# Performance work log

Hardware: AMD Instinct MI355X
Metric: run time of the kernel (lower is better)

The kernel has to match this reference:

```python
import jax, jax.numpy as jnp
import numpy as np

EMB = 1024
HEADS = 16
HEAD_DIM = EMB // HEADS


def setup_inputs() -> dict:
    key = jax.random.key(0)
    ks = jax.random.split(key, 9)
    B, T = 2, 2048
    s = 1.0 / np.sqrt(EMB)
    x = jax.random.normal(ks[0], (B, T, EMB), dtype=jnp.float32)
    Wq = jax.random.normal(ks[1], (EMB, EMB), dtype=jnp.float32) * s
    bq = jnp.zeros((EMB,), dtype=jnp.float32)
    Wk = jax.random.normal(ks[2], (EMB, EMB), dtype=jnp.float32) * s
    bk = jnp.zeros((EMB,), dtype=jnp.float32)
    Wv = jax.random.normal(ks[3], (EMB, EMB), dtype=jnp.float32) * s
    bv = jnp.zeros((EMB,), dtype=jnp.float32)
    Wo = jax.random.normal(ks[4], (EMB, EMB), dtype=jnp.float32) * s
    bo = jnp.zeros((EMB,), dtype=jnp.float32)
    return {"x": x, "Wq": Wq, "bq": bq, "Wk": Wk, "bk": bk,
            "Wv": Wv, "bv": bv, "Wo": Wo, "bo": bo}


def reference(x, Wq, bq, Wk, bk, Wv, bv, Wo, bo):
    B, T, C = x.shape
    H, D = HEADS, HEAD_DIM
    # QKV projections -> (B, H, T, D)
    q = (x @ Wq + bq).reshape(B, T, H, D).transpose(0, 2, 1, 3)
    k = (x @ Wk + bk).reshape(B, T, H, D).transpose(0, 2, 1, 3)
    v = (x @ Wv + bv).reshape(B, T, H, D).transpose(0, 2, 1, 3)
    scores = jnp.einsum('bhqd,bhkd->bhqk', q, k) / np.sqrt(D).astype(np.float32)
    causal = jnp.tril(jnp.ones((T, T), dtype=bool))  # True where allowed
    scores = jnp.where(causal, scores, -jnp.inf)
    weights = jax.nn.softmax(scores, axis=-1)  # dropout is identity at eval
    out = jnp.einsum('bhqk,bhkd->bhqd', weights, v)
    out = out.transpose(0, 2, 1, 3).reshape(B, T, C)
    return out @ Wo + bo
```

## Files before the change

### kernel.cpp

```cpp
#include <hip/hip_runtime.h>

typedef unsigned short u16;
typedef u16 u16x8 __attribute__((ext_vector_type(8)));
typedef __bf16 bf16x8 __attribute__((ext_vector_type(8)));
typedef float f32x4 __attribute__((ext_vector_type(4)));

#define EMB 1024
#define TT 2048
#define BB 2
#define NHEADS 16
#define HD 64
#define MTOT (BB * TT)

__device__ __forceinline__ u16 cvt(float f) {
  return __builtin_bit_cast(u16, (__bf16)f);
}

__device__ __forceinline__ bf16x8 asbf(u16x8 v) {
  return __builtin_bit_cast(bf16x8, v);
}

__device__ __forceinline__ void gload16(const void* g, void* l) {
  __builtin_amdgcn_global_load_lds(
      (const __attribute__((address_space(1))) void*)g,
      (__attribute__((address_space(3))) void*)l, 16, 0, 0);
}

__global__ __launch_bounds__(256) void k_prep(
    const float* __restrict__ x, u16* __restrict__ xb,
    const float* __restrict__ W0, const float* __restrict__ W1,
    const float* __restrict__ W2, const float* __restrict__ W3,
    u16* __restrict__ T0, u16* __restrict__ T1, u16* __restrict__ T2,
    u16* __restrict__ T3) {
  __shared__ float tile[32][33];
  const int bid = blockIdx.x;
  const int tid = threadIdx.x;
  if (bid >= 4096) {
    int i = (bid - 4096) * 256 + tid;
    float4 a = ((const float4*)x)[i * 2];
    float4 b = ((const float4*)x)[i * 2 + 1];
    u16x8 o;
    o[0] = cvt(a.x); o[1] = cvt(a.y); o[2] = cvt(a.z); o[3] = cvt(a.w);
    o[4] = cvt(b.x); o[5] = cvt(b.y); o[6] = cvt(b.z); o[7] = cvt(b.w);
    ((u16x8*)xb)[i] = o;
    return;
  }
  const int z = bid >> 10;
  const float* __restrict__ W = (z == 0) ? W0 : (z == 1) ? W1 : (z == 2) ? W2 : W3;
  u16* __restrict__ Wt = (z == 0) ? T0 : (z == 1) ? T1 : (z == 2) ? T2 : T3;
  const int b = bid & 1023;
  const int bx = (b & 31) * 32, by = (b >> 5) * 32;
  const int tx = tid & 31;
  const int ty = tid >> 5;
#pragma unroll
  for (int r = ty; r < 32; r += 8) tile[r][tx] = W[(by + r) * EMB + bx + tx];
  __syncthreads();
  const int tx2 = tid & 15;
  const int ty2 = tid >> 4;
#pragma unroll
  for (int r = ty2; r < 32; r += 16) {
    unsigned v = (unsigned)cvt(tile[2 * tx2][r]) |
                 ((unsigned)cvt(tile[2 * tx2 + 1][r]) << 16);
    *(unsigned*)&Wt[(bx + r) * EMB + by + 2 * tx2] = v;
  }
}

__global__ __launch_bounds__(256) void k_gemm_qkv(
    const u16* __restrict__ xb, const u16* __restrict__ WqT,
    const u16* __restrict__ WkT, const u16* __restrict__ WvT,
    const float* __restrict__ bq, const float* __restrict__ bk,
    const float* __restrict__ bv, u16* __restrict__ Q, u16* __restrict__ K,
    u16* __restrict__ Vt) {
  __shared__ u16 Al[128 * 64];
  __shared__ u16 Bl[128 * 64];
  const int tid = threadIdx.x;
  const int lane = tid & 63;
  const int w = tid >> 6;
  const int wr = w >> 1, wc = w & 1;
  const int lr = lane & 15, lg = lane >> 4;
  const int m0 = blockIdx.x * 128;
  const int nb = blockIdx.y;
  const int seg = nb >> 3;
  const int n0 = (nb & 7) * 128;
  const u16* __restrict__ Bt = (seg == 0) ? WqT : (seg == 1) ? WkT : WvT;
  const float* __restrict__ bias = (seg == 0) ? bq : (seg == 1) ? bk : bv;

  f32x4 acc[4][4];
#pragma unroll
  for (int i = 0; i < 4; i++)
#pragma unroll
    for (int j = 0; j < 4; j++) acc[i][j] = (f32x4){0.f, 0.f, 0.f, 0.f};

  const int srow = tid >> 3;
  const int sgz = ((tid >> 3) & 3) | (((tid >> 6) & 1) << 2);
  const int sc = (tid & 7) ^ sgz;
  const u16* ga0 = xb + (m0 + srow) * EMB + sc * 8;
  const u16* gb0 = Bt + (n0 + srow) * EMB + sc * 8;
  char* la0 = (char*)Al + w * 1024;
  char* lb0 = (char*)Bl + w * 1024;
  const int gfr = (lr & 3) | (((lr >> 3) & 1) << 2);

  for (int k0 = 0; k0 < EMB; k0 += 64) {
#pragma unroll
    for (int m = 0; m < 4; m++) {
      gload16(ga0 + (32 * m) * EMB + k0, la0 + m * 4096);
      gload16(gb0 + (32 * m) * EMB + k0, lb0 + m * 4096);
    }
    __syncthreads();
    u16x8 af[4][2], bfr[4][2];
#pragma unroll
    for (int hh = 0; hh < 2; hh++) {
      const int pc = ((hh * 4 + lg) ^ gfr) * 16;
#pragma unroll
      for (int mi = 0; mi < 4; mi++)
        af[mi][hh] =
            *(const u16x8*)((char*)Al + (wr * 64 + mi * 16 + lr) * 128 + pc);
#pragma unroll
      for (int ni = 0; ni < 4; ni++)
        bfr[ni][hh] =
            *(const u16x8*)((char*)Bl + (wc * 64 + ni * 16 + lr) * 128 + pc);
    }
    if (seg == 2) {
#pragma unroll
      for (int hh = 0; hh < 2; hh++)
#pragma unroll
        for (int mi = 0; mi < 4; mi++)
#pragma unroll
          for (int ni = 0; ni < 4; ni++)
            acc[mi][ni] = __builtin_amdgcn_mfma_f32_16x16x32_bf16(
                asbf(af[mi][hh]), asbf(bfr[ni][hh]), acc[mi][ni], 0, 0, 0);
    } else {
#pragma unroll
      for (int hh = 0; hh < 2; hh++)
#pragma unroll
        for (int mi = 0; mi < 4; mi++)
#pragma unroll
          for (int ni = 0; ni < 4; ni++)
            acc[mi][ni] = __builtin_amdgcn_mfma_f32_16x16x32_bf16(
                asbf(bfr[ni][hh]), asbf(af[mi][hh]), acc[mi][ni], 0, 0, 0);
    }
    __syncthreads();
  }

  const int b = m0 >> 11;
  if (seg == 2) {
#pragma unroll
    for (int ni = 0; ni < 4; ni++) {
      const int n = n0 + wc * 64 + ni * 16 + lr;
      const float bv_ = bias[n];
      const int h = n >> 6, d = n & 63;
      u16* vrow = Vt + (((b * NHEADS + h) * HD) + d) * TT;
#pragma unroll
      for (int mi = 0; mi < 4; mi++) {
        const int t0 = (m0 + wr * 64 + mi * 16 + lg * 4) & 2047;
        ushort4 pk;
        pk.x = cvt(acc[mi][ni][0] + bv_);
        pk.y = cvt(acc[mi][ni][1] + bv_);
        pk.z = cvt(acc[mi][ni][2] + bv_);
        pk.w = cvt(acc[mi][ni][3] + bv_);
        *(ushort4*)&vrow[t0] = pk;
      }
    }
  } else {
    u16* __restrict__ dst = (seg == 0) ? Q : K;
    const float qs = 0.18033688011f;
#pragma unroll
    for (int ni = 0; ni < 4; ni++) {
      const int nbase = n0 + wc * 64 + ni * 16 + lg * 4;
      const float4 bv4 = *(const float4*)&bias[nbase];
      const int h = nbase >> 6, d0 = nbase & 63;
#pragma unroll
      for (int mi = 0; mi < 4; mi++) {
        const int t = (m0 + wr * 64 + mi * 16 + lr) & 2047;
        float v0 = acc[mi][ni][0] + bv4.x;
        float v1 = acc[mi][ni][1] + bv4.y;
        float v2 = acc[mi][ni][2] + bv4.z;
        float v3 = acc[mi][ni][3] + bv4.w;
        if (seg == 0) { v0 *= qs; v1 *= qs; v2 *= qs; v3 *= qs; }
        ushort4 pk;
        pk.x = cvt(v0); pk.y = cvt(v1); pk.z = cvt(v2); pk.w = cvt(v3);
        *(ushort4*)&dst[(((b * NHEADS + h) * TT) + t) * HD + d0] = pk;
      }
    }
  }
}

__global__ __launch_bounds__(512) void k_attn(const u16* __restrict__ Q,
                                              const u16* __restrict__ Kg,
                                              const u16* __restrict__ Vt,
                                              u16* __restrict__ AO) {
  __shared__ u16 Kl[2][64 * 64];
  __shared__ u16 Vl[2][64 * 64];
  const int tid = threadIdx.x;
  const int lane = tid & 63;
  const int w = tid >> 6;
  const int lr = lane & 15, lg = lane >> 4;
  const int bh = blockIdx.x;
  const int pair = blockIdx.y;
  const int lo = pair, hi = 31 - pair;
  const int qblk = (w < 4) ? hi : lo;
  const int myend = qblk;
  const int q0 = qblk * 64 + (w & 3) * 16;
  const u16* __restrict__ Qh = Q + bh * TT * HD;
  const u16* __restrict__ Kh = Kg + bh * TT * HD;
  const u16* __restrict__ Vh = Vt + bh * HD * TT;

  const int srow = tid >> 3;
  const int sgz = ((tid >> 3) & 3) | (((tid >> 6) & 1) << 2);
  const int sc = (tid & 7) ^ sgz;

  u16x8 qf[2];
  qf[0] = *(const u16x8*)&Qh[(q0 + lr) * HD + lg * 8];
  qf[1] = *(const u16x8*)&Qh[(q0 + lr) * HD + 32 + lg * 8];

  f32x4 accO[4];
#pragma unroll
  for (int i = 0; i < 4; i++) accO[i] = (f32x4){0.f, 0.f, 0.f, 0.f};
  float mst = -__builtin_inff();
  float lsum = 0.f;

  const int nkt = hi + 1;

  gload16(Kh + srow * HD + sc * 8, (char*)Kl[0] + w * 1024);
  gload16(Vh + srow * TT + sc * 8, (char*)Vl[0] + w * 1024);
  __syncthreads();

  for (int kt = 0; kt < nkt; ++kt) {
    const int k0 = kt * 64;
    const int cur = kt & 1;
    if (kt + 1 < nkt) {
      const int kn = k0 + 64;
      gload16(Kh + (kn + srow) * HD + sc * 8, (char*)Kl[cur ^ 1] + w * 1024);
      gload16(Vh + srow * TT + kn + sc * 8, (char*)Vl[cur ^ 1] + w * 1024);
    }
    if (kt <= myend) {
      const char* Kc = (const char*)Kl[cur];
      const char* Vc = (const char*)Vl[cur];

      f32x4 s[4];
#pragma unroll
      for (int n = 0; n < 4; n++) s[n] = (f32x4){0.f, 0.f, 0.f, 0.f};
      __builtin_amdgcn_s_setprio(1);
#pragma unroll
      for (int n = 0; n < 4; n++) {
        const int kr =
            (lr & 3) + ((n & 1) << 2) + ((lr >> 2) << 3) + ((n >> 1) << 5);
        const int gg = (kr & 3) | (((kr >> 3) & 1) << 2);
#pragma unroll
        for (int dh = 0; dh < 2; dh++) {
          const int bo = ((dh * 4 + lg) ^ gg) << 4;
          u16x8 kf = *(const u16x8*)(Kc + kr * 128 + bo);
          s[n] = __builtin_amdgcn_mfma_f32_16x16x32_bf16(asbf(kf), asbf(qf[dh]),
                                                         s[n], 0, 0, 0);
        }
      }
      __builtin_amdgcn_s_setprio(0);
      if (kt == myend) {
        const int rowq = q0 + lr;
#pragma unroll
        for (int n = 0; n < 4; n++) {
          const int cb = k0 + ((n & 1) << 2) + (lg << 3) + ((n >> 1) << 5);
#pragma unroll
          for (int r = 0; r < 4; r++)
            if (cb + r > rowq) s[n][r] = -__builtin_inff();
        }
      }
      float m01 = fmaxf(fmaxf(s[0][0], s[0][1]), fmaxf(s[0][2], s[0][3]));
      float m1 = fmaxf(fmaxf(s[1][0], s[1][1]), fmaxf(s[1][2], s[1][3]));
      float m2 = fmaxf(fmaxf(s[2][0], s[2][1]), fmaxf(s[2][2], s[2][3]));
      float m3 = fmaxf(fmaxf(s[3][0], s[3][1]), fmaxf(s[3][2], s[3][3]));
      float lmax = fmaxf(fmaxf(m01, m1), fmaxf(m2, m3));
      if (!__all(lmax - mst <= 11.0f)) {
        float rm = lmax;
        rm = fmaxf(rm, __shfl_xor(rm, 16));
        rm = fmaxf(rm, __shfl_xor(rm, 32));
        float mnew = fmaxf(mst, rm);
        float corr = exp2f(mst - mnew);
        lsum *= corr;
        mst = mnew;
#pragma unroll
        for (int r = 0; r < 4; r++) {
          float ca = __shfl(corr, 20 * lg + r);
#pragma unroll
          for (int dt = 0; dt < 4; dt++) accO[dt][r] *= ca;
        }
      }
      float p[4][4];
      float ls = 0.f;
#pragma unroll
      for (int n = 0; n < 4; n++)
#pragma unroll
        for (int r = 0; r < 4; r++) {
          p[n][r] = exp2f(s[n][r] - mst);
          ls += p[n][r];
        }
      lsum += ls;
      u16x8 a1, a2;
#pragma unroll
      for (int r = 0; r < 4; r++) {
        a1[r] = cvt(p[0][r]);
        a1[4 + r] = cvt(p[1][r]);
        a2[r] = cvt(p[2][r]);
        a2[4 + r] = cvt(p[3][r]);
      }
      __builtin_amdgcn_s_setprio(1);
#pragma unroll
      for (int dt = 0; dt < 4; dt++) {
        const int row = dt * 16 + lr;
        const int gg = (row & 3) | (((row >> 3) & 1) << 2);
        const int bo0 = ((lg ^ gg) << 4);
        const int bo1 = (((4 + lg) ^ gg) << 4);
        u16x8 vf0 = *(const u16x8*)(Vc + row * 128 + bo0);
        u16x8 vf1 = *(const u16x8*)(Vc + row * 128 + bo1);
        accO[dt] = __builtin_amdgcn_mfma_f32_16x16x32_bf16(asbf(a1), asbf(vf0),
                                                           accO[dt], 0, 0, 0);
        accO[dt] = __builtin_amdgcn_mfma_f32_16x16x32_bf16(asbf(a2), asbf(vf1),
                                                           accO[dt], 0, 0, 0);
      }
      __builtin_amdgcn_s_setprio(0);
    }
    __syncthreads();
  }
  float t = lsum;
  t += __shfl_xor(t, 16);
  t += __shfl_xor(t, 32);
  float rinv = 1.0f / t;
  float ra[4];
#pragma unroll
  for (int r = 0; r < 4; r++) ra[r] = __shfl(rinv, 20 * lg + r);
  const int b = bh >> 4, h = bh & 15;
#pragma unroll
  for (int dt = 0; dt < 4; dt++)
#pragma unroll
    for (int r = 0; r < 4; r++) {
      const int row = q0 + lg * 4 + r;
      const int d = h * 64 + dt * 16 + lr;
      AO[(b * TT + row) * EMB + d] = cvt(accO[dt][r] * ra[r]);
    }
}

__global__ __launch_bounds__(256) void k_gemm_out(const u16* __restrict__ AO,
                                                  const u16* __restrict__ WoT,
                                                  const float* __restrict__ bo,
                                                  float* __restrict__ out) {
  __shared__ u16 Al[128 * 64];
  __shared__ u16 Bl[128 * 64];
  const int tid = threadIdx.x;
  const int lane = tid & 63;
  const int w = tid >> 6;
  const int wr = w >> 1, wc = w & 1;
  const int lr = lane & 15, lg = lane >> 4;
  const int m0 = blockIdx.x * 128;
  const int n0 = blockIdx.y * 128;

  f32x4 acc[4][4];
#pragma unroll
  for (int i = 0; i < 4; i++)
#pragma unroll
    for (int j = 0; j < 4; j++) acc[i][j] = (f32x4){0.f, 0.f, 0.f, 0.f};

  const int srow = tid >> 3;
  const int sgz = ((tid >> 3) & 3) | (((tid >> 6) & 1) << 2);
  const int sc = (tid & 7) ^ sgz;
  const u16* ga0 = AO + (m0 + srow) * EMB + sc * 8;
  const u16* gb0 = WoT + (n0 + srow) * EMB + sc * 8;
  char* la0 = (char*)Al + w * 1024;
  char* lb0 = (char*)Bl + w * 1024;
  const int gfr = (lr & 3) | (((lr >> 3) & 1) << 2);

  for (int k0 = 0; k0 < EMB; k0 += 64) {
#pragma unroll
    for (int m = 0; m < 4; m++) {
      gload16(ga0 + (32 * m) * EMB + k0, la0 + m * 4096);
      gload16(gb0 + (32 * m) * EMB + k0, lb0 + m * 4096);
    }
    __syncthreads();
    u16x8 af[4][2], bfr[4][2];
#pragma unroll
    for (int hh = 0; hh < 2; hh++) {
      const int pc = ((hh * 4 + lg) ^ gfr) * 16;
#pragma unroll
      for (int mi = 0; mi < 4; mi++)
        af[mi][hh] =
            *(const u16x8*)((char*)Al + (wr * 64 + mi * 16 + lr) * 128 + pc);
#pragma unroll
      for (int ni = 0; ni < 4; ni++)
        bfr[ni][hh] =
            *(const u16x8*)((char*)Bl + (wc * 64 + ni * 16 + lr) * 128 + pc);
    }
#pragma unroll
    for (int hh = 0; hh < 2; hh++)
#pragma unroll
      for (int mi = 0; mi < 4; mi++)
#pragma unroll
        for (int ni = 0; ni < 4; ni++)
          acc[mi][ni] = __builtin_amdgcn_mfma_f32_16x16x32_bf16(
              asbf(bfr[ni][hh]), asbf(af[mi][hh]), acc[mi][ni], 0, 0, 0);
    __syncthreads();
  }

#pragma unroll
  for (int ni = 0; ni < 4; ni++) {
    const int nbase = n0 + wc * 64 + ni * 16 + lg * 4;
    const float4 bv4 = *(const float4*)&bo[nbase];
#pragma unroll
    for (int mi = 0; mi < 4; mi++) {
      const int m = m0 + wr * 64 + mi * 16 + lr;
      float4 v;
      v.x = acc[mi][ni][0] + bv4.x;
      v.y = acc[mi][ni][1] + bv4.y;
      v.z = acc[mi][ni][2] + bv4.z;
      v.w = acc[mi][ni][3] + bv4.w;
      *(float4*)&out[m * EMB + nbase] = v;
    }
  }
}

extern "C" void kernel_launch(void* const* d_in, const int* in_sizes, int n_in,
                              void* d_out, int out_size, void* d_ws,
                              size_t ws_size, hipStream_t stream) {
  const float* x = (const float*)d_in[0];
  const float* Wq = (const float*)d_in[1];
  const float* bq = (const float*)d_in[2];
  const float* Wk = (const float*)d_in[3];
  const float* bk = (const float*)d_in[4];
  const float* Wv = (const float*)d_in[5];
  const float* bv = (const float*)d_in[6];
  const float* Wo = (const float*)d_in[7];
  const float* bo = (const float*)d_in[8];
  float* out = (float*)d_out;

  char* ws = (char*)d_ws;
  u16* xb = (u16*)ws;
  u16* WqT = (u16*)(ws + (8u << 20));
  u16* WkT = (u16*)(ws + (10u << 20));
  u16* WvT = (u16*)(ws + (12u << 20));
  u16* WoT = (u16*)(ws + (14u << 20));
  u16* Qb = (u16*)(ws + (16u << 20));
  u16* Kb = (u16*)(ws + (24u << 20));
  u16* Vtb = (u16*)(ws + (32u << 20));
  u16* AO = xb;

  k_prep<<<6144, 256, 0, stream>>>(x, xb, Wq, Wk, Wv, Wo, WqT, WkT, WvT, WoT);
  k_gemm_qkv<<<dim3(32, 24), 256, 0, stream>>>(xb, WqT, WkT, WvT, bq, bk, bv,
                                               Qb, Kb, Vtb);
  k_attn<<<dim3(32, 16), 512, 0, stream>>>(Qb, Kb, Vtb, AO);
  k_gemm_out<<<dim3(32, 8), 256, 0, stream>>>(AO, WoT, bo, out);
}
```

Before: 132.4 us.

## Double-buffer QKV GEMM LDS tiles with BK=32 and drop swizzle

Restructures the QKV projection GEMM main loop so the next K-slice is prefetched into a second LDS buffer while MFMAs run on the current one. The K step drops from 64 to 32 and the XOR swizzle on the LDS layout is removed. The operand order is also unified, so Q/K results now come out transposed and are stored as scalar 2-byte writes instead of ushort4 vectors. This aims to hide global-load latency, but it risks LDS bank conflicts from the unswizzled layout, uncoalesced scalar stores in the Q/K epilogue, and more barriers per unit of work.

```diff
diff --git a/kernel.cpp b/kernel.cpp
--- a/kernel.cpp
+++ b/kernel.cpp
@@ -71,8 +71,8 @@
     const float* __restrict__ bq, const float* __restrict__ bk,
     const float* __restrict__ bv, u16* __restrict__ Q, u16* __restrict__ K,
     u16* __restrict__ Vt) {
-  __shared__ u16 Al[128 * 64];
-  __shared__ u16 Bl[128 * 64];
+  __shared__ u16 Al[2][128 * 32];
+  __shared__ u16 Bl[2][128 * 32];
   const int tid = threadIdx.x;
   const int lane = tid & 63;
   const int w = tid >> 6;
@@ -91,54 +91,40 @@
 #pragma unroll
     for (int j = 0; j < 4; j++) acc[i][j] = (f32x4){0.f, 0.f, 0.f, 0.f};
 
-  const int srow = tid >> 3;
-  const int sgz = ((tid >> 3) & 3) | (((tid >> 6) & 1) << 2);
-  const int sc = (tid & 7) ^ sgz;
-  const u16* ga0 = xb + (m0 + srow) * EMB + sc * 8;
-  const u16* gb0 = Bt + (n0 + srow) * EMB + sc * 8;
-  char* la0 = (char*)Al + w * 1024;
-  char* lb0 = (char*)Bl + w * 1024;
-  const int gfr = (lr & 3) | (((lr >> 3) & 1) << 2);
-
-  for (int k0 = 0; k0 < EMB; k0 += 64) {
-#pragma unroll
-    for (int m = 0; m < 4; m++) {
-      gload16(ga0 + (32 * m) * EMB + k0, la0 + m * 4096);
-      gload16(gb0 + (32 * m) * EMB + k0, lb0 + m * 4096);
-    }
-    __syncthreads();
-    u16x8 af[4][2], bfr[4][2];
-#pragma unroll
-    for (int hh = 0; hh < 2; hh++) {
-      const int pc = ((hh * 4 + lg) ^ gfr) * 16;
-#pragma unroll
-      for (int mi = 0; mi < 4; mi++)
-        af[mi][hh] =
-            *(const u16x8*)((char*)Al + (wr * 64 + mi * 16 + lr) * 128 + pc);
+  const int srow = tid >> 2;
+  const int scol = (tid & 3) * 8;
+  const u16* ga0 = xb + (m0 + srow) * EMB + scol;
+  const u16* gb0 = Bt + (n0 + srow) * EMB + scol;
+  const int lofs = w * 1024;
+
+  gload16(ga0, (char*)Al[0] + lofs);
+  gload16(ga0 + 64 * EMB, (char*)Al[0] + lofs + 4096);
+  gload16(gb0, (char*)Bl[0] + lofs);
+  gload16(gb0 + 64 * EMB, (char*)Bl[0] + lofs + 4096);
+  __syncthreads();
+
+  int cur = 0;
+  for (int k0 = 0; k0 < EMB; k0 += 32, cur ^= 1) {
+    if (k0 + 32 < EMB) {
+      const int kn = k0 + 32;
+      gload16(ga0 + kn, (char*)Al[cur ^ 1] + lofs);
+      gload16(ga0 + 64 * EMB + kn, (char*)Al[cur ^ 1] + lofs + 4096);
+      gload16(gb0 + kn, (char*)Bl[cur ^ 1] + lofs);
+      gload16(gb0 + 64 * EMB + kn, (char*)Bl[cur ^ 1] + lofs + 4096);
+    }
+    u16x8 af[4], bfr[4];
+#pragma unroll
+    for (int mi = 0; mi < 4; mi++)
+      af[mi] = *(const u16x8*)&Al[cur][(wr * 64 + mi * 16 + lr) * 32 + lg * 8];
+#pragma unroll
+    for (int ni = 0; ni < 4; ni++)
+      bfr[ni] = *(const u16x8*)&Bl[cur][(wc * 64 + ni * 16 + lr) * 32 + lg * 8];
+#pragma unroll
+    for (int mi = 0; mi < 4; mi++)
 #pragma unroll
       for (int ni = 0; ni < 4; ni++)
-        bfr[ni][hh] =
-            *(const u16x8*)((char*)Bl + (wc * 64 + ni * 16 + lr) * 128 + pc);
-    }
-    if (seg == 2) {
-#pragma unroll
-      for (int hh = 0; hh < 2; hh++)
-#pragma unroll
-        for (int mi = 0; mi < 4; mi++)
-#pragma unroll
-          for (int ni = 0; ni < 4; ni++)
-            acc[mi][ni] = __builtin_amdgcn_mfma_f32_16x16x32_bf16(
-                asbf(af[mi][hh]), asbf(bfr[ni][hh]), acc[mi][ni], 0, 0, 0);
-    } else {
-#pragma unroll
-      for (int hh = 0; hh < 2; hh++)
-#pragma unroll
-        for (int mi = 0; mi < 4; mi++)
-#pragma unroll
-          for (int ni = 0; ni < 4; ni++)
-            acc[mi][ni] = __builtin_amdgcn_mfma_f32_16x16x32_bf16(
-                asbf(bfr[ni][hh]), asbf(af[mi][hh]), acc[mi][ni], 0, 0, 0);
-    }
+        acc[mi][ni] = __builtin_amdgcn_mfma_f32_16x16x32_bf16(
+            asbf(af[mi]), asbf(bfr[ni]), acc[mi][ni], 0, 0, 0);
     __syncthreads();
   }
 
@@ -163,23 +149,21 @@
     }
   } else {
     u16* __restrict__ dst = (seg == 0) ? Q : K;
-    const float qs = 0.18033688011f;
-#pragma unroll
-    for (int ni = 0; ni < 4; ni++) {
-      const int nbase = n0 + wc * 64 + ni * 16 + lg * 4;
-      const float4 bv4 = *(const float4*)&bias[nbase];
-      const int h = nbase >> 6, d0 = nbase & 63;
-#pragma unroll
-      for (int mi = 0; mi < 4; mi++) {
-        const int t = (m0 + wr * 64 + mi * 16 + lr) & 2047;
-        float v0 = acc[mi][ni][0] + bv4.x;
-        float v1 = acc[mi][ni][1] + bv4.y;
-        float v2 = acc[mi][ni][2] + bv4.z;
-        float v3 = acc[mi][ni][3] + bv4.w;
-        if (seg == 0) { v0 *= qs; v1 *= qs; v2 *= qs; v3 *= qs; }
-        ushort4 pk;
-        pk.x = cvt(v0); pk.y = cvt(v1); pk.z = cvt(v2); pk.w = cvt(v3);
-        *(ushort4*)&dst[(((b * NHEADS + h) * TT) + t) * HD + d0] = pk;
+    const float qs = (seg == 0) ? 0.18033688011f : 1.0f;
+#pragma unroll
+    for (int mi = 0; mi < 4; mi++) {
+      const int lmb = wr * 64 + mi * 16 + lg * 4;
+#pragma unroll
+      for (int ni = 0; ni < 4; ni++) {
+        const int n = n0 + wc * 64 + ni * 16 + lr;
+        const float bv_ = bias[n];
+        const int h = n >> 6, d = n & 63;
+#pragma unroll
+        for (int r = 0; r < 4; r++) {
+          const int t = (m0 + lmb + r) & 2047;
+          float v = (acc[mi][ni][r] + bv_) * qs;
+          dst[(((b * NHEADS + h) * TT) + t) * HD + d] = cvt(v);
+        }
       }
     }
   }
```

New measurement: 126.2 us. 1.05x faster.
